# Optimization experiments

Hardware: AMD Instinct MI355X
Metric: run time of the kernel (lower is better)

## Reference

```python
import jax, jax.numpy as jnp
import numpy as np

FX, FY, CX, CY = 320.0, 320.0, 320.0, 240.0
N_MEAS, N_MP, N_KF = 2_000_000, 100_000, 2_000


def setup_inputs() -> dict:
    key = jax.random.key(0)
    k1, k2, k3, k4 = jax.random.split(key, 4)
    tMP = jax.random.normal(k1, (N_MP, 3), jnp.float32)
    # poses: near-identity with a +5 z-translation so projective depth stays away from 0
    tKF = jnp.eye(4, dtype=jnp.float32)[None] + 0.05 * jax.random.normal(k2, (N_KF, 4, 4), jnp.float32)
    tKF = tKF.at[:, 2, 3].add(5.0)
    idxMP = jnp.arange(N_MP, dtype=jnp.int32)
    idxKF = jnp.arange(N_KF, dtype=jnp.int32)
    mKF = jax.random.randint(k3, (N_MEAS,), 0, N_KF).astype(jnp.float32)
    mMP = jax.random.randint(k4, (N_MEAS,), 0, N_MP).astype(jnp.float32)
    measurements = jnp.stack([mKF, mMP], axis=1)  # [N, 2] float ids
    return {"measurements": measurements, "tMP": tMP, "tKF": tKF, "idxMP": idxMP, "idxKF": idxKF}


def reference(measurements, tMP, tKF, idxMP, idxKF):
    # ID -> row-index join. Original does an O(N*K)/O(N*M) broadcast equality via
    # torch.where; ids here are sorted unique, so a sorted join (searchsorted)
    # yields identical indices without materializing the N x M compare.
    iKF = jnp.searchsorted(idxKF, measurements[:, 0].astype(jnp.int32))
    iMP = jnp.searchsorted(idxMP, measurements[:, 1].astype(jnp.int32))
    # homogeneous map points: [M, 4]
    tMPhomo = jnp.concatenate([tMP, jnp.ones((tMP.shape[0], 1), tMP.dtype)], axis=1)
    # gather + batched 4x4 pose @ point: [N, 4]
    pts = jnp.einsum('nij,nj->ni', tKF[iKF], tMPhomo[iMP])
    # perspective divide + intrinsics scale
    ptx = pts[:, 0] / pts[:, 2] * FX + CX
    pty = pts[:, 1] / pts[:, 2] * FY + CY
    return jnp.stack([ptx, pty], axis=1)  # [N, 2]
```

## Files before the change

kernel.cpp:

```cpp
#include <hip/hip_runtime.h>

#define FXK 320.0f
#define FYK 320.0f
#define CXK 320.0f
#define CYK 240.0f

typedef float nf4 __attribute__((ext_vector_type(4)));
typedef float float4u __attribute__((ext_vector_type(4), aligned(4)));

__global__ __launch_bounds__(256, 8) void proj_kernel(
    const nf4*    __restrict__ meas4,
    const float*  __restrict__ tMP,
    const nf4*    __restrict__ tKF4,
    nf4*          __restrict__ out4,
    const float*  __restrict__ meas,
    float*        __restrict__ out,
    int n,
    int nMPf)
{
    const int nPairs = n >> 1;
    const int stride = gridDim.x * blockDim.x;
    const int last4  = nMPf - 4;

    for (int i = blockIdx.x * blockDim.x + threadIdx.x; i < nPairs; i += stride) {
        nf4 m = __builtin_nontemporal_load(&meas4[i]);
        int kfA = (int)m.x, mpA = (int)m.y;
        int kfB = (int)m.z, mpB = (int)m.w;

        int oA = mpA * 3, oB = mpB * 3;
        int cA = oA > last4 ? last4 : oA;
        int cB = oB > last4 ? last4 : oB;
        float4u qA = *(const float4u*)(tMP + cA);
        float4u qB = *(const float4u*)(tMP + cB);
        nf4 a0 = tKF4[kfA * 4 + 0];
        nf4 a1 = tKF4[kfA * 4 + 1];
        nf4 a2 = tKF4[kfA * 4 + 2];
        nf4 b0 = tKF4[kfB * 4 + 0];
        nf4 b1 = tKF4[kfB * 4 + 1];
        nf4 b2 = tKF4[kfB * 4 + 2];

        bool sA = cA != oA, sB = cB != oB;
        float xA = sA ? qA.y : qA.x;
        float yA = sA ? qA.z : qA.y;
        float zA = sA ? qA.w : qA.z;
        float xB = sB ? qB.y : qB.x;
        float yB = sB ? qB.z : qB.y;
        float zB = sB ? qB.w : qB.z;

        float pxa = a0.x * xA + a0.y * yA + a0.z * zA + a0.w;
        float pya = a1.x * xA + a1.y * yA + a1.z * zA + a1.w;
        float pza = a2.x * xA + a2.y * yA + a2.z * zA + a2.w;
        float pxb = b0.x * xB + b0.y * yB + b0.z * zB + b0.w;
        float pyb = b1.x * xB + b1.y * yB + b1.z * zB + b1.w;
        float pzb = b2.x * xB + b2.y * yB + b2.z * zB + b2.w;
        float ia = 1.0f / pza;
        float ib = 1.0f / pzb;
        nf4 r;
        r.x = pxa * ia * FXK + CXK;
        r.y = pya * ia * FYK + CYK;
        r.z = pxb * ib * FXK + CXK;
        r.w = pyb * ib * FYK + CYK;
        __builtin_nontemporal_store(r, &out4[i]);
    }

    if ((n & 1) && blockIdx.x == 0 && threadIdx.x == 0) {
        int j = n - 1;
        int kf = (int)meas[2 * j + 0];
        int mp = (int)meas[2 * j + 1];
        float x = tMP[3 * mp + 0];
        float y = tMP[3 * mp + 1];
        float z = tMP[3 * mp + 2];
        nf4 p0 = tKF4[kf * 4 + 0];
        nf4 p1 = tKF4[kf * 4 + 1];
        nf4 p2 = tKF4[kf * 4 + 2];
        float px = p0.x * x + p0.y * y + p0.z * z + p0.w;
        float py = p1.x * x + p1.y * y + p1.z * z + p1.w;
        float pz = p2.x * x + p2.y * y + p2.z * z + p2.w;
        float inv = 1.0f / pz;
        out[2 * j + 0] = px * inv * FXK + CXK;
        out[2 * j + 1] = py * inv * FYK + CYK;
    }
}

extern "C" void kernel_launch(void* const* d_in, const int* in_sizes, int n_in,
                              void* d_out, int out_size, void* d_ws, size_t ws_size,
                              hipStream_t stream) {
    const float* meas = (const float*)d_in[0];
    const float* tMP  = (const float*)d_in[1];
    const float* tKF  = (const float*)d_in[2];

    int n    = in_sizes[0] / 2;
    int nMPf = in_sizes[1];

    int nPairs = n >> 1;
    int threads = 256;
    int blocks = (nPairs + threads - 1) / threads;
    if (blocks > 2048) blocks = 2048;
    if (blocks < 1) blocks = 1;

    proj_kernel<<<blocks, threads, 0, stream>>>(
        (const nf4*)meas, tMP, (const nf4*)tKF,
        (nf4*)d_out, meas, (float*)d_out, n, nMPf);
}
```

Baseline: 100.1 us.

## Stage first two pose rows in LDS and switch to 1024-thread blocks

Each block copies rows 0 and 1 of every keyframe pose into shared memory (64 KB) and reads them from LDS during the gather, keeping only row 2 as a global load. The block size goes from 256 to 1024 threads, the block cap is raised, and the nontemporal load/store hints are dropped. This aims to cut random global gathers of pose data, but each of up to ~977 blocks must fill 64 KB of LDS before any work starts, and the large LDS footprint limits occupancy. Poses beyond 2048 keyframes would read uninitialised LDS.

```diff
diff --git a/kernel.cpp b/kernel.cpp
--- a/kernel.cpp
+++ b/kernel.cpp
@@ -5,10 +5,12 @@
 #define CXK 320.0f
 #define CYK 240.0f
 
+#define MAX_KF 2048
+
 typedef float nf4 __attribute__((ext_vector_type(4)));
 typedef float float4u __attribute__((ext_vector_type(4), aligned(4)));
 
-__global__ __launch_bounds__(256, 8) void proj_kernel(
+__global__ __launch_bounds__(1024, 8) void proj_kernel(
     const nf4*    __restrict__ meas4,
     const float*  __restrict__ tMP,
     const nf4*    __restrict__ tKF4,
@@ -16,14 +18,24 @@
     const float*  __restrict__ meas,
     float*        __restrict__ out,
     int n,
+    int nKF,
     int nMPf)
 {
+    __shared__ nf4 sR0[MAX_KF];
+    __shared__ nf4 sR1[MAX_KF];
+    const int tid = threadIdx.x;
+    for (int p = tid; p < nKF; p += blockDim.x) {
+        sR0[p] = tKF4[p * 4 + 0];
+        sR1[p] = tKF4[p * 4 + 1];
+    }
+    __syncthreads();
+
     const int nPairs = n >> 1;
     const int stride = gridDim.x * blockDim.x;
     const int last4  = nMPf - 4;
 
-    for (int i = blockIdx.x * blockDim.x + threadIdx.x; i < nPairs; i += stride) {
-        nf4 m = __builtin_nontemporal_load(&meas4[i]);
+    for (int i = blockIdx.x * blockDim.x + tid; i < nPairs; i += stride) {
+        nf4 m = meas4[i];
         int kfA = (int)m.x, mpA = (int)m.y;
         int kfB = (int)m.z, mpB = (int)m.w;
 
@@ -32,12 +44,12 @@
         int cB = oB > last4 ? last4 : oB;
         float4u qA = *(const float4u*)(tMP + cA);
         float4u qB = *(const float4u*)(tMP + cB);
-        nf4 a0 = tKF4[kfA * 4 + 0];
-        nf4 a1 = tKF4[kfA * 4 + 1];
         nf4 a2 = tKF4[kfA * 4 + 2];
-        nf4 b0 = tKF4[kfB * 4 + 0];
-        nf4 b1 = tKF4[kfB * 4 + 1];
         nf4 b2 = tKF4[kfB * 4 + 2];
+        nf4 a0 = sR0[kfA];
+        nf4 a1 = sR1[kfA];
+        nf4 b0 = sR0[kfB];
+        nf4 b1 = sR1[kfB];
 
         bool sA = cA != oA, sB = cB != oB;
         float xA = sA ? qA.y : qA.x;
@@ -60,10 +72,10 @@
         r.y = pya * ia * FYK + CYK;
         r.z = pxb * ib * FXK + CXK;
         r.w = pyb * ib * FYK + CYK;
-        __builtin_nontemporal_store(r, &out4[i]);
+        out4[i] = r;
     }
 
-    if ((n & 1) && blockIdx.x == 0 && threadIdx.x == 0) {
+    if ((n & 1) && blockIdx.x == 0 && tid == 0) {
         int j = n - 1;
         int kf = (int)meas[2 * j + 0];
         int mp = (int)meas[2 * j + 1];
@@ -91,14 +103,16 @@
 
     int n    = in_sizes[0] / 2;
     int nMPf = in_sizes[1];
+    int nKF  = in_sizes[2] / 16;
+    if (nKF > MAX_KF) nKF = MAX_KF;
 
     int nPairs = n >> 1;
-    int threads = 256;
+    int threads = 1024;
     int blocks = (nPairs + threads - 1) / threads;
-    if (blocks > 2048) blocks = 2048;
+    if (blocks > 4096) blocks = 4096;
     if (blocks < 1) blocks = 1;
 
     proj_kernel<<<blocks, threads, 0, stream>>>(
         (const nf4*)meas, tMP, (const nf4*)tKF,
-        (nf4*)d_out, meas, (float*)d_out, n, nMPf);
+        (nf4*)d_out, meas, (float*)d_out, n, nKF, nMPf);
 }
```

Measured after the change: 93.32 us. -6.8%, faster.
